# Performance work log

Measured on AMD Instinct MI355X. Metric: run time of the kernel, lower is better.

The kernel has to match this reference:

```python
import jax, jax.numpy as jnp
import numpy as np

B = 8192       # Monte Carlo paths
NSTEP = 30     # Euler time steps
D = 100        # z_dim / number of assets
H1 = 110
H2 = 110
T = NSTEP - 1  # number of subnets
DT = np.float32(1.0 / NSTEP)
R = np.float32(0.05)   # riskfree
EPS = np.float32(1e-3) # Keras BatchNormalization epsilon


def setup_inputs() -> dict:
    key = jax.random.key(0)
    ks = jax.random.split(key, 25)
    f = jnp.float32
    X = jax.random.normal(ks[0], (B, NSTEP, D), f)
    DWs = jax.random.normal(ks[1], (B, NSTEP, D), f) * jnp.sqrt(DT)
    sigmas = jax.random.uniform(ks[2], (D,), f, 0.1, 0.4)
    y_init = jax.random.uniform(ks[3], (1,), f, 0.0, 1.0)
    z_init = jax.random.uniform(ks[4], (1, D), f, -0.1, 0.1)
    W1 = jax.random.normal(ks[5], (T, D, H1), f) / np.sqrt(D).astype(np.float32)
    W2 = jax.random.normal(ks[6], (T, H1, H2), f) / np.sqrt(H1).astype(np.float32)
    W3 = jax.random.normal(ks[7], (T, H2, D), f) / np.sqrt(H2).astype(np.float32)
    dims = [D, H1, H2, D]
    bn = {}
    for j, dim in enumerate(dims):
        bn[f"g{j}"] = 1.0 + 0.1 * jax.random.normal(ks[8 + 4 * j], (T, dim), f)
        bn[f"b{j}"] = 0.05 * jax.random.normal(ks[9 + 4 * j], (T, dim), f)
        bn[f"m{j}"] = 0.1 * jax.random.normal(ks[10 + 4 * j], (T, dim), f)
        bn[f"v{j}"] = jax.random.uniform(ks[11 + 4 * j], (T, dim), f, 0.5, 1.5)
    return dict(X=X, DWs=DWs, sigmas=sigmas, y_init=y_init, z_init=z_init,
                W1=W1, W2=W2, W3=W3, **bn)


def _bn(x, g, b, m, v):
    # Keras BatchNormalization, inference mode
    return (x - m) * jax.lax.rsqrt(v + EPS) * g + b


def _subnet(x, p):
    (w1, w2, w3, g0, b0, m0, v0, g1, b1, m1, v1,
     g2, b2, m2, v2, g3, b3, m3, v3) = p
    x = _bn(x, g0, b0, m0, v0)
    x = jax.nn.relu(x @ w1)
    x = _bn(x, g1, b1, m1, v1)
    x = jax.nn.relu(x @ w2)
    x = _bn(x, g2, b2, m2, v2)
    x = x @ w3
    return _bn(x, g3, b3, m3, v3)


def reference(X, DWs, sigmas, y_init, z_init, W1, W2, W3,
              g0, b0, m0, v0, g1, b1, m1, v1,
              g2, b2, m2, v2, g3, b3, m3, v3):
    nb = X.shape[0]
    Y0 = jnp.ones((nb, 1), X.dtype) * y_init            # [B,1]
    Z0 = jnp.ones((nb, 1), X.dtype) * z_init            # [B,D]

    def step(carry, xs):
        Y, Z = carry
        Xi, Xn, DWi, p = xs
        Y = Y + R * Y * DT + jnp.sum(sigmas * Xi * Z * DWi, axis=1, keepdims=True)
        Z = _subnet(Xn, p)
        return (Y, Z), None

    params = (W1, W2, W3, g0, b0, m0, v0, g1, b1, m1, v1,
              g2, b2, m2, v2, g3, b3, m3, v3)  # each leading dim T
    xs = (jnp.moveaxis(X[:, :T], 1, 0),        # [T,B,D]
          jnp.moveaxis(X[:, 1:T + 1], 1, 0),   # [T,B,D]
          jnp.moveaxis(DWs[:, :T], 1, 0),      # [T,B,D]
          params)
    (Y, Z), _ = jax.lax.scan(step, (Y0, Z0), xs)
    # final step: X[:,-2,:] with DWs[:,-1,:]
    Y = Y + R * Y * DT + jnp.sum(sigmas * X[:, -2, :] * Z * DWs[:, -1, :],
                                 axis=1, keepdims=True)
    return Y
```

## Files before the change

kernel.cpp:

```cpp
#include <hip/hip_runtime.h>

typedef unsigned short ushort_t;
typedef __attribute__((ext_vector_type(8))) short s16x8;
typedef __attribute__((ext_vector_type(4))) float f32x4;

#define B_PATHS 8192
#define NSTEP   30
#define DD      100
#define HH      110
#define TT      29
#define ROWSTR  3000
#define LDK     136
#define WFRAGSZ 14336
#define DT_C    (1.0f/30.0f)
#define R_C     0.05f
#define EPS_C   1e-3f

__device__ __forceinline__ ushort_t f2bf(float f) {
  unsigned u = __float_as_uint(f);
  u = u + 0x7FFFu + ((u >> 16) & 1u);
  return (ushort_t)(u >> 16);
}
__device__ __forceinline__ float bf2f(ushort_t u) {
  return __uint_as_float(((unsigned)u) << 16);
}

__global__ void prep_kernel(const float* __restrict__ W1, const float* __restrict__ W2,
                            const float* __restrict__ W3,
                            const float* g0, const float* b0, const float* m0, const float* v0,
                            const float* g1, const float* b1, const float* m1, const float* v1,
                            const float* g2, const float* b2, const float* m2, const float* v2,
                            const float* g3, const float* b3, const float* m3, const float* v3,
                            ushort_t* __restrict__ wprep, float* __restrict__ bprep)
{
  const int mat = blockIdx.x, t = blockIdx.y, tid = threadIdx.x;
  __shared__ float wsh[110*110];
  __shared__ float sin_[112], hin_[112], sout_[112], hout_[112];

  int Kr, Nr; const float* W; const float *g, *bb, *mm, *vv;
  if (mat == 0)      { Kr = 100; Nr = 110; W = W1 + t*11000; g = g0+t*100; bb = b0+t*100; mm = m0+t*100; vv = v0+t*100; }
  else if (mat == 1) { Kr = 110; Nr = 110; W = W2 + t*12100; g = g1+t*110; bb = b1+t*110; mm = m1+t*110; vv = v1+t*110; }
  else               { Kr = 110; Nr = 100; W = W3 + t*11000; g = g2+t*110; bb = b2+t*110; mm = m2+t*110; vv = v2+t*110; }

  if (tid < Kr) {
    float s = g[tid] * rsqrtf(vv[tid] + EPS_C);
    sin_[tid] = s; hin_[tid] = bb[tid] - mm[tid]*s;
  }
  if (mat == 2 && tid < Nr) {
    float s = g3[t*100+tid] * rsqrtf(v3[t*100+tid] + EPS_C);
    sout_[tid] = s; hout_[tid] = b3[t*100+tid] - m3[t*100+tid]*s;
  }
  for (int i = tid; i < Kr*Nr; i += 256) wsh[i] = W[i];
  __syncthreads();

  if (tid < 128) {
    float c = 0.f;
    if (tid < Nr) {
      for (int k = 0; k < Kr; ++k) c += hin_[k] * wsh[k*Nr + tid];
      if (mat == 2) c = c * sout_[tid] + hout_[tid];
    }
    bprep[(t*3 + mat)*128 + tid] = c;
  }

  ushort_t* wo = wprep + (size_t)(t*3 + mat) * WFRAGSZ;
  for (int ch = tid; ch < 1792; ch += 256) {
    const int lane = ch & 63, ntkb = ch >> 6;
    const int nt = ntkb % 7, kb = ntkb / 7;
    const int n  = nt*16 + (lane & 15);
    const int k0 = kb*32 + (lane >> 4)*8;
    ushort_t tmp[8];
#pragma unroll
    for (int j = 0; j < 8; ++j) {
      const int k = k0 + j;
      float v = 0.f;
      if (n < Nr && k < Kr) {
        v = sin_[k] * wsh[k*Nr + n];
        if (mat == 2) v *= sout_[n];
      }
      tmp[j] = f2bf(v);
    }
    ushort4 lo; lo.x = tmp[0]; lo.y = tmp[1]; lo.z = tmp[2]; lo.w = tmp[3];
    ushort4 hi; hi.x = tmp[4]; hi.y = tmp[5]; hi.z = tmp[6]; hi.w = tmp[7];
    *(ushort4*)(wo + ch*8)     = lo;
    *(ushort4*)(wo + ch*8 + 4) = hi;
  }
}

__device__ __forceinline__ void mlp_stage(const ushort_t* actIn, const ushort_t* __restrict__ wfrag,
                                          const float* __restrict__ biasg, ushort_t* actOut,
                                          int wr, int lane, int lrow, int quad, bool relu)
{
  f32x4 acc[7];
  const f32x4 z4 = {0.f, 0.f, 0.f, 0.f};
#pragma unroll
  for (int nt = 0; nt < 7; ++nt) acc[nt] = z4;
  s16x8 a[4];
#pragma unroll
  for (int kb = 0; kb < 4; ++kb)
    a[kb] = *(const s16x8*)(actIn + (wr + lrow)*LDK + kb*32 + quad*8);
#pragma unroll
  for (int kb = 0; kb < 4; ++kb) {
#pragma unroll
    for (int nt = 0; nt < 7; ++nt) {
      s16x8 b = *(const s16x8*)(wfrag + ((kb*7 + nt)*64 + lane)*8);
      acc[nt] = __builtin_amdgcn_mfma_f32_16x16x32_bf16(a[kb], b, acc[nt], 0, 0, 0);
    }
  }
#pragma unroll
  for (int nt = 0; nt < 7; ++nt) {
    const int col = nt*16 + lrow;
    const float bv = biasg[col];
#pragma unroll
    for (int r = 0; r < 4; ++r) {
      float u = acc[nt][r] + bv;
      if (relu) u = u > 0.f ? u : 0.f;
      actOut[(wr + quad*4 + r)*LDK + col] = f2bf(u);
    }
  }
#pragma unroll
  for (int r = 0; r < 4; ++r)
    actOut[(wr + quad*4 + r)*LDK + 112 + lrow] = 0;
}

__global__ __launch_bounds__(256, 4)
void subnet_kernel(const float* __restrict__ X, const float* __restrict__ DW,
                   const float* __restrict__ sigmas,
                   const ushort_t* __restrict__ wprep, const float* __restrict__ bprep,
                   float* __restrict__ sbuf)
{
  __shared__ __align__(16) ushort_t actA[64*LDK];
  __shared__ __align__(16) ushort_t actB[64*LDK];

  const int tid  = threadIdx.x;
  const int t    = blockIdx.y;
  const int m0   = blockIdx.x * 64;
  const int lane = tid & 63, lrow = lane & 15, quad = lane >> 4;
  const int wr   = (tid >> 6) * 16;

  for (int j = tid; j < 64*32; j += 256) {
    const int r = j >> 5, c = j & 31;
    ushort4 u; u.x = 0; u.y = 0; u.z = 0; u.w = 0;
    if (c < 25) {
      const float4 v = *(const float4*)(X + (size_t)(m0 + r)*ROWSTR + (t+1)*DD + c*4);
      u.x = f2bf(v.x); u.y = f2bf(v.y); u.z = f2bf(v.z); u.w = f2bf(v.w);
    }
    *(ushort4*)(actA + r*LDK + c*4) = u;
  }
  __syncthreads();

  const ushort_t* wf = wprep + (size_t)(t*3) * WFRAGSZ;
  const float*    bg = bprep + (t*3) * 128;

  mlp_stage(actA, wf,             bg,       actB, wr, lane, lrow, quad, true);
  __syncthreads();
  mlp_stage(actB, wf + WFRAGSZ,   bg + 128, actA, wr, lane, lrow, quad, true);
  __syncthreads();
  mlp_stage(actA, wf + 2*WFRAGSZ, bg + 256, actB, wr, lane, lrow, quad, false);
  __syncthreads();

  {
    const int row = tid >> 2, part = tid & 3;
    const int b   = m0 + row;
    const int xt  = (t == TT - 1) ? (NSTEP - 2) : (t + 1);
    const float* xr = X  + (size_t)b*ROWSTR + xt*DD;
    const float* dr = DW + (size_t)b*ROWSTR + (t+1)*DD;
    float p = 0.f;
#pragma unroll
    for (int g = part; g < 25; g += 4) {
      const float4 xv = *(const float4*)(xr + g*4);
      const float4 dv = *(const float4*)(dr + g*4);
      const float4 sg = *(const float4*)(sigmas + g*4);
      const ushort4 zu = *(const ushort4*)(actB + row*LDK + g*4);
      p += sg.x*xv.x*dv.x*bf2f(zu.x);
      p += sg.y*xv.y*dv.y*bf2f(zu.y);
      p += sg.z*xv.z*dv.z*bf2f(zu.z);
      p += sg.w*xv.w*dv.w*bf2f(zu.w);
    }
    p += __shfl_xor(p, 1, 64);
    p += __shfl_xor(p, 2, 64);
    if (part == 0)
      sbuf[(size_t)(t+1)*B_PATHS + b] = p;
  }
}

__global__ void y_kernel(const float* __restrict__ X, const float* __restrict__ DW,
                         const float* __restrict__ sigmas, const float* __restrict__ y_init,
                         const float* __restrict__ z_init, const float* __restrict__ sbuf,
                         float* __restrict__ out)
{
  const int b = blockIdx.x * blockDim.x + threadIdx.x;
  const float* xr = X + (size_t)b * ROWSTR;
  const float* dr = DW + (size_t)b * ROWSTR;
  float s0 = 0.f;
#pragma unroll 5
  for (int c = 0; c < 25; ++c) {
    float4 xv = *(const float4*)(xr + c*4);
    float4 dv = *(const float4*)(dr + c*4);
    float4 sg = *(const float4*)(sigmas + c*4);
    float4 zv = *(const float4*)(z_init + c*4);
    s0 += sg.x*xv.x*zv.x*dv.x;
    s0 += sg.y*xv.y*zv.y*dv.y;
    s0 += sg.z*xv.z*zv.z*dv.z;
    s0 += sg.w*xv.w*zv.w*dv.w;
  }
  float y = y_init[0];
  y = y + R_C*y*DT_C + s0;
#pragma unroll
  for (int tau = 1; tau < NSTEP; ++tau)
    y = y + R_C*y*DT_C + sbuf[(size_t)tau*B_PATHS + b];
  out[b] = y;
}

extern "C" void kernel_launch(void* const* d_in, const int* in_sizes, int n_in,
                              void* d_out, int out_size, void* d_ws, size_t ws_size,
                              hipStream_t stream) {
  const float* X      = (const float*)d_in[0];
  const float* DWs    = (const float*)d_in[1];
  const float* sigmas = (const float*)d_in[2];
  const float* y_init = (const float*)d_in[3];
  const float* z_init = (const float*)d_in[4];
  const float* W1     = (const float*)d_in[5];
  const float* W2     = (const float*)d_in[6];
  const float* W3     = (const float*)d_in[7];
  const float* bn[16];
  for (int i = 0; i < 16; ++i) bn[i] = (const float*)d_in[8 + i];

  char* ws = (char*)d_ws;
  ushort_t* wprep = (ushort_t*)ws;
  float*    bprep = (float*)(ws + 2494464);
  float*    sbuf  = (float*)(ws + 2539008);
  float*    out   = (float*)d_out;

  prep_kernel<<<dim3(3, TT), 256, 0, stream>>>(
      W1, W2, W3,
      bn[0], bn[1], bn[2], bn[3],  bn[4], bn[5], bn[6], bn[7],
      bn[8], bn[9], bn[10], bn[11], bn[12], bn[13], bn[14], bn[15],
      wprep, bprep);
  subnet_kernel<<<dim3(B_PATHS/64, TT), 256, 0, stream>>>(
      X, DWs, sigmas, wprep, bprep, sbuf);
  y_kernel<<<dim3(B_PATHS/256), 256, 0, stream>>>(
      X, DWs, sigmas, y_init, z_init, sbuf, out);
}
```

Measured before the change: 334.3 us.

## Give each wave 32 rows to reuse weight fragments, drop block barriers

```diff
diff --git a/kernel.cpp b/kernel.cpp
--- a/kernel.cpp
+++ b/kernel.cpp
@@ -86,129 +86,146 @@
   }
 }
 
-__device__ __forceinline__ void mlp_stage(const ushort_t* actIn, const ushort_t* __restrict__ wfrag,
-                                          const float* __restrict__ biasg, ushort_t* actOut,
-                                          int wr, int lane, int lrow, int quad, bool relu)
-{
-  f32x4 acc[7];
+__device__ __forceinline__ void mlp_stage32(ushort_t* act, const ushort_t* __restrict__ wfrag,
+                                            const float* __restrict__ biasg,
+                                            int wrow, int lane, int lrow, int quad, bool relu)
+{
+  f32x4 acc[7][2];
   const f32x4 z4 = {0.f, 0.f, 0.f, 0.f};
 #pragma unroll
-  for (int nt = 0; nt < 7; ++nt) acc[nt] = z4;
-  s16x8 a[4];
-#pragma unroll
-  for (int kb = 0; kb < 4; ++kb)
-    a[kb] = *(const s16x8*)(actIn + (wr + lrow)*LDK + kb*32 + quad*8);
+  for (int nt = 0; nt < 7; ++nt) { acc[nt][0] = z4; acc[nt][1] = z4; }
+
 #pragma unroll
   for (int kb = 0; kb < 4; ++kb) {
+    const s16x8 a0 = *(const s16x8*)(act + (wrow      + lrow)*LDK + kb*32 + quad*8);
+    const s16x8 a1 = *(const s16x8*)(act + (wrow + 16 + lrow)*LDK + kb*32 + quad*8);
+    s16x8 b[7];
+#pragma unroll
+    for (int nt = 0; nt < 7; ++nt)
+      b[nt] = *(const s16x8*)(wfrag + ((kb*7 + nt)*64 + lane)*8);
 #pragma unroll
     for (int nt = 0; nt < 7; ++nt) {
-      s16x8 b = *(const s16x8*)(wfrag + ((kb*7 + nt)*64 + lane)*8);
-      acc[nt] = __builtin_amdgcn_mfma_f32_16x16x32_bf16(a[kb], b, acc[nt], 0, 0, 0);
-    }
-  }
+      acc[nt][0] = __builtin_amdgcn_mfma_f32_16x16x32_bf16(a0, b[nt], acc[nt][0], 0, 0, 0);
+      acc[nt][1] = __builtin_amdgcn_mfma_f32_16x16x32_bf16(a1, b[nt], acc[nt][1], 0, 0, 0);
+    }
+  }
+
 #pragma unroll
   for (int nt = 0; nt < 7; ++nt) {
     const int col = nt*16 + lrow;
     const float bv = biasg[col];
 #pragma unroll
-    for (int r = 0; r < 4; ++r) {
-      float u = acc[nt][r] + bv;
-      if (relu) u = u > 0.f ? u : 0.f;
-      actOut[(wr + quad*4 + r)*LDK + col] = f2bf(u);
-    }
-  }
-#pragma unroll
-  for (int r = 0; r < 4; ++r)
-    actOut[(wr + quad*4 + r)*LDK + 112 + lrow] = 0;
-}
-
-__global__ __launch_bounds__(256, 4)
+    for (int mh = 0; mh < 2; ++mh) {
+#pragma unroll
+      for (int r = 0; r < 4; ++r) {
+        float u = acc[nt][mh][r] + bv;
+        if (relu) u = u > 0.f ? u : 0.f;
+        act[(wrow + mh*16 + quad*4 + r)*LDK + col] = f2bf(u);
+      }
+    }
+  }
+#pragma unroll
+  for (int mh = 0; mh < 2; ++mh)
+#pragma unroll
+    for (int r = 0; r < 4; ++r)
+      act[(wrow + mh*16 + quad*4 + r)*LDK + 112 + lrow] = 0;
+}
+
+__global__ __launch_bounds__(128, 4)
 void subnet_kernel(const float* __restrict__ X, const float* __restrict__ DW,
                    const float* __restrict__ sigmas,
                    const ushort_t* __restrict__ wprep, const float* __restrict__ bprep,
                    float* __restrict__ sbuf)
 {
-  __shared__ __align__(16) ushort_t actA[64*LDK];
-  __shared__ __align__(16) ushort_t actB[64*LDK];
+  __shared__ __align__(16) ushort_t act[64*LDK];
 
   const int tid  = threadIdx.x;
   const int t    = blockIdx.y;
   const int m0   = blockIdx.x * 64;
-  const int lane = tid & 63, lrow = lane & 15, quad = lane >> 4;
-  const int wr   = (tid >> 6) * 16;
-
-  for (int j = tid; j < 64*32; j += 256) {
-    const int r = j >> 5, c = j & 31;
-    ushort4 u; u.x = 0; u.y = 0; u.z = 0; u.w = 0;
-    if (c < 25) {
-      const float4 v = *(const float4*)(X + (size_t)(m0 + r)*ROWSTR + (t+1)*DD + c*4);
-      u.x = f2bf(v.x); u.y = f2bf(v.y); u.z = f2bf(v.z); u.w = f2bf(v.w);
-    }
-    *(ushort4*)(actA + r*LDK + c*4) = u;
-  }
-  __syncthreads();
+  const int lane = tid & 63;
+  const int wrow = (tid >> 6) * 32;
+  const int lrow = lane & 15, quad = lane >> 4;
+
+  {
+    const int c  = lane & 31;
+    const int r0 = lane >> 5;
+#pragma unroll
+    for (int i = 0; i < 16; ++i) {
+      const int r = r0 + i*2;
+      ushort4 u; u.x = 0; u.y = 0; u.z = 0; u.w = 0;
+      if (c < 25) {
+        const float4 v = *(const float4*)(X + (size_t)(m0 + wrow + r)*ROWSTR + (t+1)*DD + c*4);
+        u.x = f2bf(v.x); u.y = f2bf(v.y); u.z = f2bf(v.z); u.w = f2bf(v.w);
+      }
+      *(ushort4*)(act + (wrow + r)*LDK + c*4) = u;
+    }
+  }
 
   const ushort_t* wf = wprep + (size_t)(t*3) * WFRAGSZ;
   const float*    bg = bprep + (t*3) * 128;
 
-  mlp_stage(actA, wf,             bg,       actB, wr, lane, lrow, quad, true);
-  __syncthreads();
-  mlp_stage(actB, wf + WFRAGSZ,   bg + 128, actA, wr, lane, lrow, quad, true);
-  __syncthreads();
-  mlp_stage(actA, wf + 2*WFRAGSZ, bg + 256, actB, wr, lane, lrow, quad, false);
-  __syncthreads();
+  mlp_stage32(act, wf,             bg,       wrow, lane, lrow, quad, true);
+  mlp_stage32(act, wf + WFRAGSZ,   bg + 128, wrow, lane, lrow, quad, true);
+  mlp_stage32(act, wf + 2*WFRAGSZ, bg + 256, wrow, lane, lrow, quad, false);
 
   {
-    const int row = tid >> 2, part = tid & 3;
-    const int b   = m0 + row;
-    const int xt  = (t == TT - 1) ? (NSTEP - 2) : (t + 1);
+    const int row  = wrow + (lane >> 1);
+    const int part = lane & 1;
+    const int b    = m0 + row;
+    const int xt   = (t == TT - 1) ? (NSTEP - 2) : (t + 1);
     const float* xr = X  + (size_t)b*ROWSTR + xt*DD;
     const float* dr = DW + (size_t)b*ROWSTR + (t+1)*DD;
     float p = 0.f;
 #pragma unroll
-    for (int g = part; g < 25; g += 4) {
+    for (int g = part; g < 25; g += 2) {
       const float4 xv = *(const float4*)(xr + g*4);
       const float4 dv = *(const float4*)(dr + g*4);
       const float4 sg = *(const float4*)(sigmas + g*4);
-      const ushort4 zu = *(const ushort4*)(actB + row*LDK + g*4);
+      const ushort4 zu = *(const ushort4*)(act + row*LDK + g*4);
       p += sg.x*xv.x*dv.x*bf2f(zu.x);
       p += sg.y*xv.y*dv.y*bf2f(zu.y);
       p += sg.z*xv.z*dv.z*bf2f(zu.z);
       p += sg.w*xv.w*dv.w*bf2f(zu.w);
     }
     p += __shfl_xor(p, 1, 64);
-    p += __shfl_xor(p, 2, 64);
     if (part == 0)
       sbuf[(size_t)(t+1)*B_PATHS + b] = p;
   }
 }
 
-__global__ void y_kernel(const float* __restrict__ X, const float* __restrict__ DW,
-                         const float* __restrict__ sigmas, const float* __restrict__ y_init,
-                         const float* __restrict__ z_init, const float* __restrict__ sbuf,
-                         float* __restrict__ out)
-{
-  const int b = blockIdx.x * blockDim.x + threadIdx.x;
+__global__ __launch_bounds__(256)
+void y_kernel(const float* __restrict__ X, const float* __restrict__ DW,
+              const float* __restrict__ sigmas, const float* __restrict__ y_init,
+              const float* __restrict__ z_init, const float* __restrict__ sbuf,
+              float* __restrict__ out)
+{
+  const int tid  = threadIdx.x;
+  const int row  = tid >> 2, part = tid & 3;
+  const int b    = blockIdx.x * 64 + row;
   const float* xr = X + (size_t)b * ROWSTR;
   const float* dr = DW + (size_t)b * ROWSTR;
-  float s0 = 0.f;
-#pragma unroll 5
-  for (int c = 0; c < 25; ++c) {
-    float4 xv = *(const float4*)(xr + c*4);
-    float4 dv = *(const float4*)(dr + c*4);
-    float4 sg = *(const float4*)(sigmas + c*4);
-    float4 zv = *(const float4*)(z_init + c*4);
-    s0 += sg.x*xv.x*zv.x*dv.x;
-    s0 += sg.y*xv.y*zv.y*dv.y;
-    s0 += sg.z*xv.z*zv.z*dv.z;
-    s0 += sg.w*xv.w*zv.w*dv.w;
-  }
-  float y = y_init[0];
-  y = y + R_C*y*DT_C + s0;
-#pragma unroll
-  for (int tau = 1; tau < NSTEP; ++tau)
-    y = y + R_C*y*DT_C + sbuf[(size_t)tau*B_PATHS + b];
-  out[b] = y;
+  float p = 0.f;
+#pragma unroll
+  for (int g = part; g < 25; g += 4) {
+    const float4 xv = *(const float4*)(xr + g*4);
+    const float4 dv = *(const float4*)(dr + g*4);
+    const float4 sg = *(const float4*)(sigmas + g*4);
+    const float4 zv = *(const float4*)(z_init + g*4);
+    p += sg.x*xv.x*zv.x*dv.x;
+    p += sg.y*xv.y*zv.y*dv.y;
+    p += sg.z*xv.z*zv.z*dv.z;
+    p += sg.w*xv.w*zv.w*dv.w;
+  }
+  p += __shfl_xor(p, 1, 64);
+  p += __shfl_xor(p, 2, 64);
+  if (part == 0) {
+    float y = y_init[0];
+    y = y + R_C*y*DT_C + p;
+#pragma unroll
+    for (int tau = 1; tau < NSTEP; ++tau)
+      y = y + R_C*y*DT_C + sbuf[(size_t)tau*B_PATHS + b];
+    out[b] = y;
+  }
 }
 
 extern "C" void kernel_launch(void* const* d_in, const int* in_sizes, int n_in,
@@ -236,8 +253,8 @@
       bn[0], bn[1], bn[2], bn[3],  bn[4], bn[5], bn[6], bn[7],
       bn[8], bn[9], bn[10], bn[11], bn[12], bn[13], bn[14], bn[15],
       wprep, bprep);
-  subnet_kernel<<<dim3(B_PATHS/64, TT), 256, 0, stream>>>(
+  subnet_kernel<<<dim3(B_PATHS/64, TT), 128, 0, stream>>>(
       X, DWs, sigmas, wprep, bprep, sbuf);
-  y_kernel<<<dim3(B_PATHS/256), 256, 0, stream>>>(
+  y_kernel<<<dim3(B_PATHS/64), 256, 0, stream>>>(
       X, DWs, sigmas, y_init, z_init, sbuf, out);
 }
```

Result: slower. 348.8 us (+4.3%).
